# Performance work log

Measured on AMD Instinct MI355X. Metric: run time of the kernel, lower is better.

## Reference

```python
import jax, jax.numpy as jnp
import numpy as np

DIM = 256
HEADS = 8
HD = DIM // HEADS  # 32
RPE_H = 512
STRIDE = 16
B, NQ = 4, 300
HH, WW = 64, 64
N = HH * WW


def setup_inputs() -> dict:
    key = jax.random.key(0)
    ks = jax.random.split(key, 24)

    def lin(k, fan_in, fan_out):
        return (jax.random.normal(k, (fan_in, fan_out), jnp.float32)
                / np.float32(np.sqrt(fan_in)))

    # boxes in absolute pixel coords (image is WW*STRIDE = 1024 px wide)
    rp_xy = jax.random.uniform(ks[0], (B, NQ, 1, 2), jnp.float32) * (WW * STRIDE)
    rp_wh = jax.random.uniform(ks[1], (B, NQ, 1, 2), jnp.float32) * 256.0 + 16.0
    reference_points = jnp.concatenate([rp_xy, rp_wh], axis=-1)  # [B,NQ,1,4]

    inp = {
        "query": jax.random.normal(ks[2], (B, NQ, DIM), jnp.float32),
        "reference_points": reference_points,
        "k_input_flatten": jax.random.normal(ks[3], (B, N, DIM), jnp.float32),
        "v_input_flatten": jax.random.normal(ks[4], (B, N, DIM), jnp.float32),
        "input_spatial_shapes": jnp.array([[HH, WW]], dtype=jnp.int32),
        "input_padding_mask": (jax.random.uniform(ks[5], (B, N)) < 0.1).astype(jnp.int32),
        # projections (stored as [in, out]; y = x @ W + b)
        "Wq": lin(ks[6], DIM, DIM), "bq": jnp.zeros((DIM,), jnp.float32),
        "Wk": lin(ks[7], DIM, DIM), "bk": jnp.zeros((DIM,), jnp.float32),
        "Wv": lin(ks[8], DIM, DIM), "bv": jnp.zeros((DIM,), jnp.float32),
        "Wp": lin(ks[9], DIM, DIM), "bp": jnp.zeros((DIM,), jnp.float32),
        # CPB MLP 1 (x-deltas): Linear(2,512)+ReLU+Linear(512,HEADS,no bias)
        "W1x": lin(ks[10], 2, RPE_H), "b1x": jnp.zeros((RPE_H,), jnp.float32),
        "W2x": lin(ks[11], RPE_H, HEADS),
        # CPB MLP 2 (y-deltas)
        "W1y": lin(ks[12], 2, RPE_H), "b1y": jnp.zeros((RPE_H,), jnp.float32),
        "W2y": lin(ks[13], RPE_H, HEADS),
    }
    return inp


def reference(query, reference_points, k_input_flatten, v_input_flatten,
              input_spatial_shapes, input_padding_mask,
              Wq, bq, Wk, bk, Wv, bv, Wp, bp,
              W1x, b1x, W2x, W1y, b1y, W2y):
    h = int(input_spatial_shapes[0, 0])
    w = int(input_spatial_shapes[0, 1])
    scale = HD ** -0.5

    # cxcywh -> (x1,y1,x2,y2)
    c, s = reference_points[..., :2], reference_points[..., 2:]
    ref_pts = jnp.concatenate([c - s / 2, c + s / 2], axis=-1)  # [B,NQ,1,4]

    pos_x = (jnp.arange(w, dtype=jnp.float32) + 0.5) * STRIDE  # [w]
    pos_y = (jnp.arange(h, dtype=jnp.float32) + 0.5) * STRIDE  # [h]
    delta_x = ref_pts[..., 0::2] - pos_x[None, None, :, None]  # [B,NQ,w,2]
    delta_y = ref_pts[..., 1::2] - pos_y[None, None, :, None]  # [B,NQ,h,2]

    rpe_x = jax.nn.relu(delta_x @ W1x + b1x) @ W2x  # [B,NQ,w,HEADS]
    rpe_y = jax.nn.relu(delta_y @ W1y + b1y) @ W2y  # [B,NQ,h,HEADS]
    rpe = rpe_x[:, :, None, :, :] + rpe_y[:, :, :, None, :]  # [B,NQ,h,w,H]

    Bq, Nq, C = query.shape
    rpe = rpe.reshape(Bq, Nq, h * w, HEADS).transpose(0, 3, 1, 2)  # [B,H,NQ,N]

    q = (query @ Wq + bq).reshape(Bq, Nq, HEADS, HD).transpose(0, 2, 1, 3) * scale
    k = (k_input_flatten @ Wk + bk).reshape(Bq, -1, HEADS, HD).transpose(0, 2, 1, 3)
    v = (v_input_flatten @ Wv + bv).reshape(Bq, -1, HEADS, HD).transpose(0, 2, 1, 3)

    attn = jnp.einsum('bhqd,bhkd->bhqk', q, k) + rpe
    attn = attn + input_padding_mask[:, None, None, :].astype(attn.dtype) * (-100.0)
    fi = jnp.finfo(attn.dtype)
    attn = jnp.clip(attn, fi.min, fi.max)
    attn = jax.nn.softmax(attn, axis=-1)

    x = jnp.einsum('bhqk,bhkd->bhqd', attn, v)
    x = x.transpose(0, 2, 1, 3).reshape(Bq, Nq, C)
    return x @ Wp + bp
```

## Files before the change

kernel.cpp:

```cpp
#include <hip/hip_runtime.h>
#include <math.h>

#define B_   4
#define NQ_  300
#define DIM_ 256
#define H_   8
#define HD_  32
#define N_   4096

typedef _Float16 f16;
typedef f16   f16x8 __attribute__((ext_vector_type(8)));
typedef f16   f16x4 __attribute__((ext_vector_type(4)));
typedef float f32x4 __attribute__((ext_vector_type(4)));

__global__ __launch_bounds__(256) void prep_wt(
    const float* __restrict__ Wq, const float* __restrict__ Wk,
    const float* __restrict__ Wv, const float* __restrict__ Wp,
    f16* __restrict__ WT, float qscale)
{
  __shared__ float t[64][65];
  const int z = blockIdx.z;
  const float* W = z == 0 ? Wq : z == 1 ? Wk : z == 2 ? Wv : Wp;
  const float s = z == 0 ? qscale : 1.0f;
  f16* O = WT + (size_t)z * 65536;
  const int k0 = blockIdx.y * 64, n0 = blockIdx.x * 64;
  const int r = threadIdx.x >> 2, c0 = (threadIdx.x & 3) * 16;
#pragma unroll
  for (int c = 0; c < 16; c += 4) {
    float4 v = *(const float4*)(W + (size_t)(k0 + r) * 256 + n0 + c0 + c);
    t[r][c0 + c] = v.x; t[r][c0 + c + 1] = v.y;
    t[r][c0 + c + 2] = v.z; t[r][c0 + c + 3] = v.w;
  }
  __syncthreads();
  f16* orow = O + (size_t)(n0 + r) * 256 + k0 + c0;
#pragma unroll
  for (int c = 0; c < 16; c += 4) {
    f16x4 p;
    p[0] = (f16)(t[c0 + c + 0][r] * s);
    p[1] = (f16)(t[c0 + c + 1][r] * s);
    p[2] = (f16)(t[c0 + c + 2][r] * s);
    p[3] = (f16)(t[c0 + c + 3][r] * s);
    *(f16x4*)(orow + c) = p;
  }
}

__device__ __forceinline__ void gemm_body(
    const void* __restrict__ Ain, const f16* __restrict__ WT,
    const float* __restrict__ bias, void* __restrict__ C,
    int M, float scale, int a_f16, int mode, int bm, int bn, int tid)
{
  __shared__ f16 As[64][40];
  __shared__ f16 Bs[64][40];
  const int lane = tid & 63;
  const int wv = tid >> 6;
  const int l15 = lane & 15, g = lane >> 4;
  const int arow = tid >> 2, akq = (tid & 3) * 8;

  f32x4 acc[4];
#pragma unroll
  for (int nt = 0; nt < 4; ++nt) acc[nt] = (f32x4){0.f, 0.f, 0.f, 0.f};

  for (int k0 = 0; k0 < 256; k0 += 32) {
    {
      const int gm = bm + arow;
      f16x8 av;
      if (gm < M) {
        if (a_f16) {
          av = *(const f16x8*)((const f16*)Ain + (size_t)gm * 256 + k0 + akq);
        } else {
          const float* ap = (const float*)Ain + (size_t)gm * 256 + k0 + akq;
          float4 a0 = *(const float4*)ap;
          float4 a1 = *(const float4*)(ap + 4);
          av[0] = (f16)a0.x; av[1] = (f16)a0.y; av[2] = (f16)a0.z; av[3] = (f16)a0.w;
          av[4] = (f16)a1.x; av[5] = (f16)a1.y; av[6] = (f16)a1.z; av[7] = (f16)a1.w;
        }
      } else {
#pragma unroll
        for (int i = 0; i < 8; ++i) av[i] = (f16)0.f;
      }
      *(f16x8*)&As[arow][akq] = av;
      *(f16x8*)&Bs[arow][akq] =
          *(const f16x8*)(WT + (size_t)(bn + arow) * 256 + k0 + akq);
    }
    __syncthreads();
    const f16x8 af = *(const f16x8*)&As[wv * 16 + l15][g * 8];
#pragma unroll
    for (int nt = 0; nt < 4; ++nt) {
      const f16x8 bf = *(const f16x8*)&Bs[nt * 16 + l15][g * 8];
      acc[nt] = __builtin_amdgcn_mfma_f32_16x16x32_f16(af, bf, acc[nt], 0, 0, 0);
    }
    __syncthreads();
  }

#pragma unroll
  for (int nt = 0; nt < 4; ++nt) {
    const int n = bn + nt * 16 + l15;
    const float bv = bias[n] * scale;
    if (mode == 2) {
      const int m0 = bm + wv * 16 + g * 4;
      const int bb = m0 >> 12, nk = m0 & 4095;
      f16x4 pk;
#pragma unroll
      for (int r = 0; r < 4; ++r) pk[r] = (f16)(acc[nt][r] + bv);
      *(f16x4*)((f16*)C + (size_t)bb * (256 * 4096) + (size_t)n * 4096 + nk) = pk;
    } else {
#pragma unroll
      for (int r = 0; r < 4; ++r) {
        const int m = bm + wv * 16 + g * 4 + r;
        if (m >= M) continue;
        const float v = acc[nt][r] + bv;
        if (mode == 0) ((float*)C)[(size_t)m * 256 + n] = v;
        else           ((f16*)C)[(size_t)m * 256 + n] = (f16)v;
      }
    }
  }
}

__global__ __launch_bounds__(256) void proj_qkv(
    const float* __restrict__ query, const float* __restrict__ kin,
    const float* __restrict__ vin, const f16* __restrict__ WT,
    const float* __restrict__ bq, const float* __restrict__ bk,
    const float* __restrict__ bv, f16* __restrict__ Qf,
    f16* __restrict__ Kf, f16* __restrict__ Vtf, float qscale)
{
  const int z = blockIdx.z;
  const int bm = blockIdx.y * 64, bn = blockIdx.x * 64;
  if (z == 0) {
    if (bm >= B_ * NQ_) return;
    gemm_body(query, WT, bq, Qf, B_ * NQ_, qscale, 0, 1, bm, bn, threadIdx.x);
  } else if (z == 1) {
    gemm_body(kin, WT + 65536, bk, Kf, B_ * N_, 1.0f, 0, 1, bm, bn, threadIdx.x);
  } else {
    gemm_body(vin, WT + 2 * 65536, bv, Vtf, B_ * N_, 1.0f, 0, 2, bm, bn, threadIdx.x);
  }
}

__global__ __launch_bounds__(256) void gemm_out(
    const f16* __restrict__ X, const f16* __restrict__ WT,
    const float* __restrict__ bp, float* __restrict__ out)
{
  gemm_body(X, WT + 3 * 65536, bp, out, B_ * NQ_, 1.0f, 1, 0,
            blockIdx.y * 64, blockIdx.x * 64, threadIdx.x);
}

__global__ __launch_bounds__(256) void rpe_kernel(
    const float* __restrict__ refpts,
    const float* __restrict__ W1x, const float* __restrict__ b1x, const float* __restrict__ W2x,
    const float* __restrict__ W1y, const float* __restrict__ b1y, const float* __restrict__ W2y,
    float* __restrict__ rpx, float* __restrict__ rpy)
{
  __shared__ float sRed[4][64][8];
  const int tid = threadIdx.x;
  const int lane = tid & 63;
  const int wv = __builtin_amdgcn_readfirstlane(tid >> 6);
  const int bq = blockIdx.x;
  const int axis = blockIdx.y;
  const float* W1 = axis ? W1y : W1x;
  const float* b1 = axis ? b1y : b1x;
  const float* W2 = axis ? W2y : W2x;
  float* out = axis ? rpy : rpx;

  const float c  = refpts[bq * 4 + axis];
  const float sz = refpts[bq * 4 + 2 + axis];
  const float pos = (lane + 0.5f) * 16.0f;
  const float d0 = c - 0.5f * sz - pos;
  const float d1 = c + 0.5f * sz - pos;
  float acc[8] = {};
  const int r0 = wv * 128;
#pragma unroll 4
  for (int i = 0; i < 128; ++i) {
    const int r = r0 + i;
    const float w10 = W1[r], w11 = W1[512 + r], bb = b1[r];
    const float hv = fmaxf(fmaf(d0, w10, fmaf(d1, w11, bb)), 0.0f);
    const float* w2r = W2 + r * 8;
#pragma unroll
    for (int hh = 0; hh < 8; ++hh) acc[hh] += hv * w2r[hh];
  }
#pragma unroll
  for (int hh = 0; hh < 8; ++hh) sRed[wv][lane][hh] = acc[hh];
  __syncthreads();
  for (int idx = tid; idx < 512; idx += 256) {
    const int jj = idx >> 3, hh = idx & 7;
    out[(size_t)bq * 512 + idx] =
        sRed[0][jj][hh] + sRed[1][jj][hh] + sRed[2][jj][hh] + sRed[3][jj][hh];
  }
}

__global__ __launch_bounds__(512) void attn_mfma(
    const f16* __restrict__ Qf, const f16* __restrict__ Kf,
    const f16* __restrict__ Vtf, const float* __restrict__ rpx,
    const float* __restrict__ rpy, const int* __restrict__ mask,
    f16* __restrict__ X)
{
  __shared__ float smask[N_];
  __shared__ float srx[16][68];
  __shared__ float sry[16][68];
  __shared__ float mO[7][8][64];
  __shared__ float mlm[7][16];
  __shared__ float mll[7][16];

  const int tid = threadIdx.x;
  const int lane = tid & 63;
  const int kh = tid >> 6;
  const int qb = blockIdx.x % 20;
  const int h  = (blockIdx.x / 20) % H_;
  const int b  = blockIdx.x / (20 * H_);
  const int q0 = qb * 16;
  const float L2E = 1.44269504f;

  {
    const int4* mm4 = (const int4*)(mask + b * N_);
    for (int i = tid; i < N_ / 4; i += 512) {
      int4 mm = mm4[i];
      smask[4 * i + 0] = -100.f * L2E * (float)mm.x;
      smask[4 * i + 1] = -100.f * L2E * (float)mm.y;
      smask[4 * i + 2] = -100.f * L2E * (float)mm.z;
      smask[4 * i + 3] = -100.f * L2E * (float)mm.w;
    }
  }
  for (int i = tid; i < 1024; i += 512) {
    int qq = i >> 6, j = i & 63;
    int qg = q0 + qq; if (qg > NQ_ - 1) qg = NQ_ - 1;
    size_t base = (size_t)(b * NQ_ + qg) * 512 + (size_t)j * 8 + h;
    srx[qq][j] = rpx[base] * L2E;
    sry[qq][j] = rpy[base] * L2E;
  }
  __syncthreads();

  const int l15 = lane & 15, g = lane >> 4;
  const int qrow = q0 + l15;
  const int qq = qrow > NQ_ - 1 ? NQ_ - 1 : qrow;

  const f16x8 qf = *(const f16x8*)(Qf + (size_t)(b * NQ_ + qq) * 256 + h * 32 + g * 8);

  f32x4 O0 = {0.f, 0.f, 0.f, 0.f}, O1 = {0.f, 0.f, 0.f, 0.f};
  float lacc = 0.f;
  float mrun = -1e30f;
  const f16* kb  = Kf + (size_t)b * N_ * 256 + h * 32 + g * 8;
  const f16* v0p = Vtf + (size_t)(b * 256 + h * 32 + l15) * N_ + g * 4;
  const f16* v1p = v0p + (size_t)16 * N_;

  for (int sp = 0; sp < 4; ++sp) {
    const int kbase = kh * 512 + sp * 128;
    f32x4 s2c[8];
    float lmax = -1e30f;
#pragma unroll
    for (int cc = 0; cc < 8; ++cc) {
      const int k0 = kbase + cc * 16;
      f16x8 kf = *(const f16x8*)(kb + (size_t)(k0 + l15) * 256);
      f32x4 S = __builtin_amdgcn_mfma_f32_16x16x32_f16(
          kf, qf, (f32x4){0.f, 0.f, 0.f, 0.f}, 0, 0, 0);
      const float ry2 = sry[l15][k0 >> 6];
      const float4 rx = *(const float4*)&srx[l15][(k0 & 63) + g * 4];
      const float4 sm = *(const float4*)&smask[k0 + g * 4];
      f32x4 s2;
      s2[0] = fmaf(S[0], L2E, rx.x + sm.x + ry2);
      s2[1] = fmaf(S[1], L2E, rx.y + sm.y + ry2);
      s2[2] = fmaf(S[2], L2E, rx.z + sm.z + ry2);
      s2[3] = fmaf(S[3], L2E, rx.w + sm.w + ry2);
      lmax = fmaxf(lmax, fmaxf(fmaxf(s2[0], s2[1]), fmaxf(s2[2], s2[3])));
      s2c[cc] = s2;
    }
    lmax = fmaxf(lmax, __shfl_xor(lmax, 16));
    lmax = fmaxf(lmax, __shfl_xor(lmax, 32));
    const float mnew = fmaxf(mrun, lmax);
    const float f = exp2f(mrun - mnew);
    mrun = mnew;
    lacc *= f;
#pragma unroll
    for (int r = 0; r < 4; ++r) { O0[r] *= f; O1[r] *= f; }
#pragma unroll
    for (int cc = 0; cc < 8; ++cc) {
      const int k0 = kbase + cc * 16;
      f16x4 pf;
      float ls = 0.f;
#pragma unroll
      for (int r = 0; r < 4; ++r) {
        const float pv = exp2f(s2c[cc][r] - mrun);
        ls += pv;
        pf[r] = (f16)pv;
      }
      lacc += ls;
      const f16x4 vf0 = *(const f16x4*)(v0p + k0);
      const f16x4 vf1 = *(const f16x4*)(v1p + k0);
      O0 = __builtin_amdgcn_mfma_f32_16x16x16f16(vf0, pf, O0, 0, 0, 0);
      O1 = __builtin_amdgcn_mfma_f32_16x16x16f16(vf1, pf, O1, 0, 0, 0);
    }
  }

  lacc += __shfl_xor(lacc, 16);
  lacc += __shfl_xor(lacc, 32);

  if (kh > 0) {
#pragma unroll
    for (int r = 0; r < 4; ++r) {
      mO[kh - 1][r][lane] = O0[r];
      mO[kh - 1][4 + r][lane] = O1[r];
    }
    if (lane < 16) {
      mlm[kh - 1][lane] = mrun;
      mll[kh - 1][lane] = lacc;
    }
  }
  __syncthreads();
  if (kh == 0) {
    float ms = mrun;
#pragma unroll
    for (int w = 0; w < 7; ++w) ms = fmaxf(ms, mlm[w][l15]);
    const float f0 = exp2f(mrun - ms);
    float lt = lacc * f0;
    float fw[7];
#pragma unroll
    for (int w = 0; w < 7; ++w) {
      fw[w] = exp2f(mlm[w][l15] - ms);
      lt += mll[w][l15] * fw[w];
    }
    const float rl = 1.0f / lt;
    if (qrow < NQ_) {
      f16* xr = X + (size_t)(b * NQ_ + qrow) * 256 + h * 32;
      f16x4 p0, p1;
#pragma unroll
      for (int r = 0; r < 4; ++r) {
        float o0 = O0[r] * f0, o1 = O1[r] * f0;
#pragma unroll
        for (int w = 0; w < 7; ++w) {
          o0 += mO[w][r][lane] * fw[w];
          o1 += mO[w][4 + r][lane] * fw[w];
        }
        p0[r] = (f16)(o0 * rl);
        p1[r] = (f16)(o1 * rl);
      }
      *(f16x4*)(xr + g * 4) = p0;
      *(f16x4*)(xr + 16 + g * 4) = p1;
    }
  }
}

extern "C" void kernel_launch(void* const* d_in, const int* in_sizes, int n_in,
                              void* d_out, int out_size, void* d_ws, size_t ws_size,
                              hipStream_t stream)
{
  const float* query  = (const float*)d_in[0];
  const float* refpts = (const float*)d_in[1];
  const float* kin    = (const float*)d_in[2];
  const float* vin    = (const float*)d_in[3];
  const int*   mask   = (const int*)d_in[5];
  const float* Wq = (const float*)d_in[6];
  const float* bq = (const float*)d_in[7];
  const float* Wk = (const float*)d_in[8];
  const float* bk = (const float*)d_in[9];
  const float* Wv = (const float*)d_in[10];
  const float* bv = (const float*)d_in[11];
  const float* Wp = (const float*)d_in[12];
  const float* bp = (const float*)d_in[13];
  const float* W1x = (const float*)d_in[14];
  const float* b1x = (const float*)d_in[15];
  const float* W2x = (const float*)d_in[16];
  const float* W1y = (const float*)d_in[17];
  const float* b1y = (const float*)d_in[18];
  const float* W2y = (const float*)d_in[19];

  char* wsb = (char*)d_ws;
  f16*   Qf  = (f16*)(wsb);
  f16*   Kf  = (f16*)(wsb + 622592);
  f16*   Vtf = (f16*)(wsb + 9011200);
  float* rpx = (float*)(wsb + 17399808);
  float* rpy = (float*)(wsb + 19857408);
  f16*   X   = (f16*)(wsb + 22315008);
  f16*   WT  = (f16*)(wsb + 22937600);

  const float scale = 0.17677669529663687f;

  hipLaunchKernelGGL(prep_wt, dim3(4, 4, 4), dim3(256), 0, stream,
                     Wq, Wk, Wv, Wp, WT, scale);
  hipLaunchKernelGGL(rpe_kernel, dim3(B_ * NQ_, 2), dim3(256), 0, stream,
                     refpts, W1x, b1x, W2x, W1y, b1y, W2y, rpx, rpy);
  hipLaunchKernelGGL(proj_qkv, dim3(4, 256, 3), dim3(256), 0, stream,
                     query, kin, vin, WT, bq, bk, bv, Qf, Kf, Vtf, scale);
  hipLaunchKernelGGL(attn_mfma, dim3(B_ * H_ * 20), dim3(512), 0, stream,
                     Qf, Kf, Vtf, rpx, rpy, mask, X);
  hipLaunchKernelGGL(gemm_out, dim3(4, 19), dim3(256), 0, stream,
                     X, WT, bp, (float*)d_out);
}
```

Before: 242.3 us.

## Process two 16-query tiles per attention block to reuse K/V loads

Each attention block now handles 32 queries as two 16-row MFMA tiles, so every K and V fragment loaded from global memory feeds twice as many MFMAs. The key chunk per softmax step shrinks from 128 to 64, and the K/V fragments for a chunk are loaded up front to overlap the loads with compute. The grid halves to 320 blocks, which lowers parallelism on a large GPU, and register and shared-memory use grow, which may reduce occupancy.

Result: faster. 223.0 us (-8.0%).

```diff
diff --git a/kernel.cpp b/kernel.cpp
--- a/kernel.cpp
+++ b/kernel.cpp
@@ -193,19 +193,19 @@
     f16* __restrict__ X)
 {
   __shared__ float smask[N_];
-  __shared__ float srx[16][68];
-  __shared__ float sry[16][68];
-  __shared__ float mO[7][8][64];
-  __shared__ float mlm[7][16];
-  __shared__ float mll[7][16];
+  __shared__ float srx[32][68];
+  __shared__ float sry[32][68];
+  __shared__ float mO[7][2][8][64];
+  __shared__ float mlm[7][32];
+  __shared__ float mll[7][32];
 
   const int tid = threadIdx.x;
   const int lane = tid & 63;
   const int kh = tid >> 6;
-  const int qb = blockIdx.x % 20;
-  const int h  = (blockIdx.x / 20) % H_;
-  const int b  = blockIdx.x / (20 * H_);
-  const int q0 = qb * 16;
+  const int qg = blockIdx.x % 10;
+  const int h  = (blockIdx.x / 10) % H_;
+  const int b  = blockIdx.x / (10 * H_);
+  const int q0 = qg * 32;
   const float L2E = 1.44269504f;
 
   {
@@ -218,120 +218,155 @@
       smask[4 * i + 3] = -100.f * L2E * (float)mm.w;
     }
   }
-  for (int i = tid; i < 1024; i += 512) {
+  for (int i = tid; i < 2048; i += 512) {
     int qq = i >> 6, j = i & 63;
-    int qg = q0 + qq; if (qg > NQ_ - 1) qg = NQ_ - 1;
-    size_t base = (size_t)(b * NQ_ + qg) * 512 + (size_t)j * 8 + h;
+    int qg2 = q0 + qq; if (qg2 > NQ_ - 1) qg2 = NQ_ - 1;
+    size_t base = (size_t)(b * NQ_ + qg2) * 512 + (size_t)j * 8 + h;
     srx[qq][j] = rpx[base] * L2E;
     sry[qq][j] = rpy[base] * L2E;
   }
   __syncthreads();
 
   const int l15 = lane & 15, g = lane >> 4;
-  const int qrow = q0 + l15;
-  const int qq = qrow > NQ_ - 1 ? NQ_ - 1 : qrow;
-
-  const f16x8 qf = *(const f16x8*)(Qf + (size_t)(b * NQ_ + qq) * 256 + h * 32 + g * 8);
-
-  f32x4 O0 = {0.f, 0.f, 0.f, 0.f}, O1 = {0.f, 0.f, 0.f, 0.f};
-  float lacc = 0.f;
-  float mrun = -1e30f;
+  const int qrow0 = q0 + l15;
+  const int qrow1 = q0 + 16 + l15;
+  const int qa = qrow0 > NQ_ - 1 ? NQ_ - 1 : qrow0;
+  const int qbq = qrow1 > NQ_ - 1 ? NQ_ - 1 : qrow1;
+
+  const f16x8 qf0 = *(const f16x8*)(Qf + (size_t)(b * NQ_ + qa) * 256 + h * 32 + g * 8);
+  const f16x8 qf1 = *(const f16x8*)(Qf + (size_t)(b * NQ_ + qbq) * 256 + h * 32 + g * 8);
+
+  f32x4 O00 = {0.f,0.f,0.f,0.f}, O01 = {0.f,0.f,0.f,0.f};
+  f32x4 O10 = {0.f,0.f,0.f,0.f}, O11 = {0.f,0.f,0.f,0.f};
+  float lacc0 = 0.f, lacc1 = 0.f;
+  float mrun0 = -1e30f, mrun1 = -1e30f;
   const f16* kb  = Kf + (size_t)b * N_ * 256 + h * 32 + g * 8;
   const f16* v0p = Vtf + (size_t)(b * 256 + h * 32 + l15) * N_ + g * 4;
   const f16* v1p = v0p + (size_t)16 * N_;
 
-  for (int sp = 0; sp < 4; ++sp) {
-    const int kbase = kh * 512 + sp * 128;
-    f32x4 s2c[8];
-    float lmax = -1e30f;
-#pragma unroll
-    for (int cc = 0; cc < 8; ++cc) {
+  for (int sp = 0; sp < 8; ++sp) {
+    const int kbase = kh * 512 + sp * 64;
+    f16x8 kf[4];
+    f16x4 va[4], vb[4];
+#pragma unroll
+    for (int cc = 0; cc < 4; ++cc) {
+      kf[cc] = *(const f16x8*)(kb + (size_t)(kbase + cc * 16 + l15) * 256);
+      va[cc] = *(const f16x4*)(v0p + kbase + cc * 16);
+      vb[cc] = *(const f16x4*)(v1p + kbase + cc * 16);
+    }
+    f32x4 s0[4], s1[4];
+    float lm0 = -1e30f, lm1 = -1e30f;
+#pragma unroll
+    for (int cc = 0; cc < 4; ++cc) {
       const int k0 = kbase + cc * 16;
-      f16x8 kf = *(const f16x8*)(kb + (size_t)(k0 + l15) * 256);
-      f32x4 S = __builtin_amdgcn_mfma_f32_16x16x32_f16(
-          kf, qf, (f32x4){0.f, 0.f, 0.f, 0.f}, 0, 0, 0);
-      const float ry2 = sry[l15][k0 >> 6];
-      const float4 rx = *(const float4*)&srx[l15][(k0 & 63) + g * 4];
+      f32x4 S0 = __builtin_amdgcn_mfma_f32_16x16x32_f16(
+          kf[cc], qf0, (f32x4){0.f,0.f,0.f,0.f}, 0, 0, 0);
+      f32x4 S1 = __builtin_amdgcn_mfma_f32_16x16x32_f16(
+          kf[cc], qf1, (f32x4){0.f,0.f,0.f,0.f}, 0, 0, 0);
+      const float ry0 = sry[l15][k0 >> 6];
+      const float ry1 = sry[16 + l15][k0 >> 6];
+      const float4 rx0 = *(const float4*)&srx[l15][(k0 & 63) + g * 4];
+      const float4 rx1 = *(const float4*)&srx[16 + l15][(k0 & 63) + g * 4];
       const float4 sm = *(const float4*)&smask[k0 + g * 4];
-      f32x4 s2;
-      s2[0] = fmaf(S[0], L2E, rx.x + sm.x + ry2);
-      s2[1] = fmaf(S[1], L2E, rx.y + sm.y + ry2);
-      s2[2] = fmaf(S[2], L2E, rx.z + sm.z + ry2);
-      s2[3] = fmaf(S[3], L2E, rx.w + sm.w + ry2);
-      lmax = fmaxf(lmax, fmaxf(fmaxf(s2[0], s2[1]), fmaxf(s2[2], s2[3])));
-      s2c[cc] = s2;
-    }
-    lmax = fmaxf(lmax, __shfl_xor(lmax, 16));
-    lmax = fmaxf(lmax, __shfl_xor(lmax, 32));
-    const float mnew = fmaxf(mrun, lmax);
-    const float f = exp2f(mrun - mnew);
-    mrun = mnew;
-    lacc *= f;
-#pragma unroll
-    for (int r = 0; r < 4; ++r) { O0[r] *= f; O1[r] *= f; }
-#pragma unroll
-    for (int cc = 0; cc < 8; ++cc) {
-      const int k0 = kbase + cc * 16;
-      f16x4 pf;
-      float ls = 0.f;
+      s0[cc][0] = fmaf(S0[0], L2E, rx0.x + sm.x + ry0);
+      s0[cc][1] = fmaf(S0[1], L2E, rx0.y + sm.y + ry0);
+      s0[cc][2] = fmaf(S0[2], L2E, rx0.z + sm.z + ry0);
+      s0[cc][3] = fmaf(S0[3], L2E, rx0.w + sm.w + ry0);
+      s1[cc][0] = fmaf(S1[0], L2E, rx1.x + sm.x + ry1);
+      s1[cc][1] = fmaf(S1[1], L2E, rx1.y + sm.y + ry1);
+      s1[cc][2] = fmaf(S1[2], L2E, rx1.z + sm.z + ry1);
+      s1[cc][3] = fmaf(S1[3], L2E, rx1.w + sm.w + ry1);
+      lm0 = fmaxf(lm0, fmaxf(fmaxf(s0[cc][0], s0[cc][1]), fmaxf(s0[cc][2], s0[cc][3])));
+      lm1 = fmaxf(lm1, fmaxf(fmaxf(s1[cc][0], s1[cc][1]), fmaxf(s1[cc][2], s1[cc][3])));
+    }
+    lm0 = fmaxf(lm0, __shfl_xor(lm0, 16));
+    lm0 = fmaxf(lm0, __shfl_xor(lm0, 32));
+    lm1 = fmaxf(lm1, __shfl_xor(lm1, 16));
+    lm1 = fmaxf(lm1, __shfl_xor(lm1, 32));
+    const float mn0 = fmaxf(mrun0, lm0);
+    const float mn1 = fmaxf(mrun1, lm1);
+    const float f0 = exp2f(mrun0 - mn0);
+    const float f1 = exp2f(mrun1 - mn1);
+    mrun0 = mn0; mrun1 = mn1;
+    lacc0 *= f0; lacc1 *= f1;
+#pragma unroll
+    for (int r = 0; r < 4; ++r) {
+      O00[r] *= f0; O01[r] *= f0;
+      O10[r] *= f1; O11[r] *= f1;
+    }
+#pragma unroll
+    for (int cc = 0; cc < 4; ++cc) {
+      f16x4 pf0, pf1;
 #pragma unroll
       for (int r = 0; r < 4; ++r) {
-        const float pv = exp2f(s2c[cc][r] - mrun);
-        ls += pv;
-        pf[r] = (f16)pv;
+        const float p0 = exp2f(s0[cc][r] - mrun0);
+        const float p1 = exp2f(s1[cc][r] - mrun1);
+        lacc0 += p0; lacc1 += p1;
+        pf0[r] = (f16)p0; pf1[r] = (f16)p1;
       }
-      lacc += ls;
-      const f16x4 vf0 = *(const f16x4*)(v0p + k0);
-      const f16x4 vf1 = *(const f16x4*)(v1p + k0);
-      O0 = __builtin_amdgcn_mfma_f32_16x16x16f16(vf0, pf, O0, 0, 0, 0);
-      O1 = __builtin_amdgcn_mfma_f32_16x16x16f16(vf1, pf, O1, 0, 0, 0);
-    }
-  }
-
-  lacc += __shfl_xor(lacc, 16);
-  lacc += __shfl_xor(lacc, 32);
+      O00 = __builtin_amdgcn_mfma_f32_16x16x16f16(va[cc], pf0, O00, 0, 0, 0);
+      O01 = __builtin_amdgcn_mfma_f32_16x16x16f16(vb[cc], pf0, O01, 0, 0, 0);
+      O10 = __builtin_amdgcn_mfma_f32_16x16x16f16(va[cc], pf1, O10, 0, 0, 0);
+      O11 = __builtin_amdgcn_mfma_f32_16x16x16f16(vb[cc], pf1, O11, 0, 0, 0);
+    }
+  }
+
+  lacc0 += __shfl_xor(lacc0, 16); lacc0 += __shfl_xor(lacc0, 32);
+  lacc1 += __shfl_xor(lacc1, 16); lacc1 += __shfl_xor(lacc1, 32);
 
   if (kh > 0) {
 #pragma unroll
     for (int r = 0; r < 4; ++r) {
-      mO[kh - 1][r][lane] = O0[r];
-      mO[kh - 1][4 + r][lane] = O1[r];
+      mO[kh - 1][0][r][lane]     = O00[r];
+      mO[kh - 1][0][4 + r][lane] = O01[r];
+      mO[kh - 1][1][r][lane]     = O10[r];
+      mO[kh - 1][1][4 + r][lane] = O11[r];
     }
     if (lane < 16) {
-      mlm[kh - 1][lane] = mrun;
-      mll[kh - 1][lane] = lacc;
+      mlm[kh - 1][lane]      = mrun0;
+      mlm[kh - 1][16 + lane] = mrun1;
+      mll[kh - 1][lane]      = lacc0;
+      mll[kh - 1][16 + lane] = lacc1;
     }
   }
   __syncthreads();
   if (kh == 0) {
-    float ms = mrun;
-#pragma unroll
-    for (int w = 0; w < 7; ++w) ms = fmaxf(ms, mlm[w][l15]);
-    const float f0 = exp2f(mrun - ms);
-    float lt = lacc * f0;
-    float fw[7];
-#pragma unroll
-    for (int w = 0; w < 7; ++w) {
-      fw[w] = exp2f(mlm[w][l15] - ms);
-      lt += mll[w][l15] * fw[w];
-    }
-    const float rl = 1.0f / lt;
-    if (qrow < NQ_) {
-      f16* xr = X + (size_t)(b * NQ_ + qrow) * 256 + h * 32;
-      f16x4 p0, p1;
-#pragma unroll
-      for (int r = 0; r < 4; ++r) {
-        float o0 = O0[r] * f0, o1 = O1[r] * f0;
-#pragma unroll
-        for (int w = 0; w < 7; ++w) {
-          o0 += mO[w][r][lane] * fw[w];
-          o1 += mO[w][4 + r][lane] * fw[w];
+#pragma unroll
+    for (int qt = 0; qt < 2; ++qt) {
+      const float mr = qt ? mrun1 : mrun0;
+      const float la = qt ? lacc1 : lacc0;
+      const f32x4 Oa = qt ? O10 : O00;
+      const f32x4 Ob = qt ? O11 : O01;
+      float ms = mr;
+#pragma unroll
+      for (int w = 0; w < 7; ++w) ms = fmaxf(ms, mlm[w][qt * 16 + l15]);
+      const float fme = exp2f(mr - ms);
+      float lt = la * fme;
+      float fw[7];
+#pragma unroll
+      for (int w = 0; w < 7; ++w) {
+        fw[w] = exp2f(mlm[w][qt * 16 + l15] - ms);
+        lt += mll[w][qt * 16 + l15] * fw[w];
+      }
+      const float rl = 1.0f / lt;
+      const int qrow = qt ? qrow1 : qrow0;
+      if (qrow < NQ_) {
+        f16* xr = X + (size_t)(b * NQ_ + qrow) * 256 + h * 32;
+        f16x4 p0, p1;
+#pragma unroll
+        for (int r = 0; r < 4; ++r) {
+          float o0 = Oa[r] * fme, o1 = Ob[r] * fme;
+#pragma unroll
+          for (int w = 0; w < 7; ++w) {
+            o0 += mO[w][qt][r][lane] * fw[w];
+            o1 += mO[w][qt][4 + r][lane] * fw[w];
+          }
+          p0[r] = (f16)(o0 * rl);
+          p1[r] = (f16)(o1 * rl);
         }
-        p0[r] = (f16)(o0 * rl);
-        p1[r] = (f16)(o1 * rl);
+        *(f16x4*)(xr + g * 4) = p0;
+        *(f16x4*)(xr + 16 + g * 4) = p1;
       }
-      *(f16x4*)(xr + g * 4) = p0;
-      *(f16x4*)(xr + 16 + g * 4) = p1;
     }
   }
 }
@@ -377,7 +412,7 @@
                      refpts, W1x, b1x, W2x, W1y, b1y, W2y, rpx, rpy);
   hipLaunchKernelGGL(proj_qkv, dim3(4, 256, 3), dim3(256), 0, stream,
                      query, kin, vin, WT, bq, bk, bv, Qf, Kf, Vtf, scale);
-  hipLaunchKernelGGL(attn_mfma, dim3(B_ * H_ * 20), dim3(512), 0, stream,
+  hipLaunchKernelGGL(attn_mfma, dim3(B_ * H_ * 10), dim3(512), 0, stream,
                      Qf, Kf, Vtf, rpx, rpy, mask, X);
   hipLaunchKernelGGL(gemm_out, dim3(4, 19), dim3(256), 0, stream,
                      X, WT, bp, (float*)d_out);
```
